# Kernel tuning notes

Hardware: AMD Instinct MI355X
Metric: run time of the kernel (lower is better)

## Reference

```python
import jax, jax.numpy as jnp
import numpy as np

B, D, C = 16384, 2048, 1000  # batch, in_features (feature dim), out_features (classes)
INIT_SCALE = 10.0
EPS = 1e-12


def setup_inputs() -> dict:
    key = jax.random.key(0)
    k1, k2 = jax.random.split(key)
    x = jax.random.normal(k1, (B, D), dtype=jnp.float32)
    weights = jax.random.normal(k2, (C, D), dtype=jnp.float32)  # prototypes
    scales = jnp.ones((1,), dtype=jnp.float32) * INIT_SCALE
    return {"x": x, "weights": weights, "scales": scales}


def reference(x, weights, scales):
    # Pairwise Euclidean distance between features [B,D] and prototypes [C,D]
    x2 = jnp.sum(x * x, axis=-1, keepdims=True)            # [B,1]
    w2 = jnp.sum(weights * weights, axis=-1)               # [C]
    cross = jnp.einsum('bd,cd->bc', x, weights)            # [B,C]
    d2 = jnp.maximum(x2 + w2[None, :] - 2.0 * cross, EPS)  # clamp for sqrt stability
    distances = jnp.sqrt(d2)                               # [B,C]
    logits = -scales * distances  # dml forward: -self.learn(distances)
    return logits
```

## Files before the change

### kernel.cpp

```cpp
#include <hip/hip_runtime.h>
#include <hip/hip_bf16.h>
#include <stdint.h>

#define B_ROWS 16384
#define D_K    2048
#define C_COLS 1000
#define C_PAD  1024
#define EPS_D2 1e-12f

typedef __attribute__((ext_vector_type(8))) short bf16x8;
typedef __attribute__((ext_vector_type(4))) float f32x4;

__device__ __forceinline__ unsigned short f2bf_rne(float f) {
    union { float f; uint32_t u; } a; a.f = f;
    uint32_t u = a.u;
    uint32_t r = (u + 0x7FFFu + ((u >> 16) & 1u)) >> 16;
    return (unsigned short)r;
}

__device__ __forceinline__ void async16(void* lds, const void* g) {
    __builtin_amdgcn_global_load_lds(
        (const __attribute__((address_space(1))) unsigned int*)g,
        (__attribute__((address_space(3))) unsigned int*)lds,
        16, 0, 0);
}

__global__ void prep_kernel(const float* __restrict__ x, const float* __restrict__ w,
                            __hip_bfloat16* __restrict__ xb, __hip_bfloat16* __restrict__ wb,
                            float* __restrict__ x2, float* __restrict__ w2) {
    const int row = blockIdx.x;
    const int t = threadIdx.x;

    const float* src;
    __hip_bfloat16* dst;
    float* norm_out;
    bool valid;
    if (row < B_ROWS) {
        src = x + (size_t)row * D_K;
        dst = xb + (size_t)row * D_K;
        norm_out = x2 + row;
        valid = true;
    } else {
        int c = row - B_ROWS;
        src = w + (size_t)c * D_K;
        dst = wb + (size_t)c * D_K;
        norm_out = w2 + c;
        valid = (c < C_COLS);
    }

    float4 v0, v1;
    if (valid) {
        const float4* s4 = (const float4*)src;
        v0 = s4[t];
        v1 = s4[t + 256];
    } else {
        v0 = make_float4(0.f, 0.f, 0.f, 0.f);
        v1 = v0;
    }

    float ss = v0.x*v0.x + v0.y*v0.y + v0.z*v0.z + v0.w*v0.w
             + v1.x*v1.x + v1.y*v1.y + v1.z*v1.z + v1.w*v1.w;

    uint2 p0, p1;
    p0.x = (uint32_t)f2bf_rne(v0.x) | ((uint32_t)f2bf_rne(v0.y) << 16);
    p0.y = (uint32_t)f2bf_rne(v0.z) | ((uint32_t)f2bf_rne(v0.w) << 16);
    p1.x = (uint32_t)f2bf_rne(v1.x) | ((uint32_t)f2bf_rne(v1.y) << 16);
    p1.y = (uint32_t)f2bf_rne(v1.z) | ((uint32_t)f2bf_rne(v1.w) << 16);
    ((uint2*)dst)[t]       = p0;
    ((uint2*)dst)[t + 256] = p1;

    #pragma unroll
    for (int off = 32; off > 0; off >>= 1) ss += __shfl_down(ss, off, 64);
    __shared__ float wsum[4];
    if ((t & 63) == 0) wsum[t >> 6] = ss;
    __syncthreads();
    if (t == 0) *norm_out = wsum[0] + wsum[1] + wsum[2] + wsum[3];
}

__global__ __launch_bounds__(256) void dml_gemm(
    const __hip_bfloat16* __restrict__ A,
    const __hip_bfloat16* __restrict__ Bm,
    const float* __restrict__ x2, const float* __restrict__ w2,
    const float* __restrict__ scales, float* __restrict__ out)
{
    __shared__ __align__(16) __hip_bfloat16 lsA[128 * 32];
    __shared__ __align__(16) __hip_bfloat16 lsB[128 * 32];

    const int tid  = threadIdx.x;
    const int wave = tid >> 6;
    const int lane = tid & 63;
    const int m0 = blockIdx.y * 128;
    const int n0 = blockIdx.x * 128;
    const int wm = wave >> 1;
    const int wn = wave & 1;

    const int srow = wave * 32 + (lane >> 2);
    const int scol = (lane & 3) * 8;
    const __hip_bfloat16* gA0 = A  + (size_t)(m0 + srow) * D_K + scol;
    const __hip_bfloat16* gA1 = gA0 + (size_t)16 * D_K;
    const __hip_bfloat16* gB0 = Bm + (size_t)(n0 + srow) * D_K + scol;
    const __hip_bfloat16* gB1 = gB0 + (size_t)16 * D_K;
    char* lA0 = (char*)lsA + wave * 32 * 64 + lane * 16;
    char* lA1 = lA0 + 16 * 64;
    char* lB0 = (char*)lsB + wave * 32 * 64 + lane * 16;
    char* lB1 = lB0 + 16 * 64;

    const int fr = lane & 15;
    const int fq = lane >> 4;
    const __hip_bfloat16* fA = lsA + (wm * 64 + fr) * 32 + fq * 8;
    const __hip_bfloat16* fB = lsB + (wn * 64 + fr) * 32 + fq * 8;

    f32x4 acc[4][4] = {};

    for (int k0 = 0; k0 < D_K; k0 += 32) {
        __syncthreads();
        async16(lA0, gA0); async16(lA1, gA1);
        async16(lB0, gB0); async16(lB1, gB1);
        gA0 += 32; gA1 += 32; gB0 += 32; gB1 += 32;
        __syncthreads();

        bf16x8 a[4], b[4];
        #pragma unroll
        for (int i = 0; i < 4; i++) a[i] = *(const bf16x8*)(fA + i * 16 * 32);
        #pragma unroll
        for (int j = 0; j < 4; j++) b[j] = *(const bf16x8*)(fB + j * 16 * 32);
        #pragma unroll
        for (int i = 0; i < 4; i++)
            #pragma unroll
            for (int j = 0; j < 4; j++)
                acc[i][j] = __builtin_amdgcn_mfma_f32_16x16x32_bf16(a[i], b[j], acc[i][j], 0, 0, 0);
    }

    const float s = scales[0];
    const int colb = n0 + wn * 64 + fr;
    const int rowb = m0 + wm * 64 + fq * 4;

    float xv[4][4];
    #pragma unroll
    for (int i = 0; i < 4; i++)
        #pragma unroll
        for (int r = 0; r < 4; r++)
            xv[i][r] = x2[rowb + i * 16 + r];

    #pragma unroll
    for (int j = 0; j < 4; j++) {
        const int gn = colb + j * 16;
        const bool nok = (gn < C_COLS);
        const float w2v = nok ? w2[gn] : 0.f;
        #pragma unroll
        for (int i = 0; i < 4; i++) {
            const int gm = rowb + i * 16;
            #pragma unroll
            for (int r = 0; r < 4; r++) {
                float d2 = xv[i][r] + w2v - 2.0f * acc[i][j][r];
                d2 = fmaxf(d2, EPS_D2);
                float val = -s * __builtin_sqrtf(d2);
                if (nok) out[(size_t)(gm + r) * C_COLS + gn] = val;
            }
        }
    }
}

extern "C" void kernel_launch(void* const* d_in, const int* in_sizes, int n_in,
                              void* d_out, int out_size, void* d_ws, size_t ws_size,
                              hipStream_t stream) {
    const float* x      = (const float*)d_in[0];
    const float* w      = (const float*)d_in[1];
    const float* scales = (const float*)d_in[2];
    float* out = (float*)d_out;

    char* ws = (char*)d_ws;
    __hip_bfloat16* xb = (__hip_bfloat16*)ws;
    __hip_bfloat16* wb = (__hip_bfloat16*)(ws + (size_t)B_ROWS * D_K * 2);
    float* x2 = (float*)(ws + (size_t)B_ROWS * D_K * 2 + (size_t)C_PAD * D_K * 2);
    float* w2 = x2 + B_ROWS;

    prep_kernel<<<dim3(B_ROWS + C_PAD), dim3(256), 0, stream>>>(x, w, xb, wb, x2, w2);
    dml_gemm<<<dim3(C_PAD / 128, B_ROWS / 128), dim3(256), 0, stream>>>(xb, wb, x2, w2, scales, out);
}
```

Before: 327.5 us.

## Swizzle LDS tiles, remap blocks per XCD, and use one wave per prep row

Adds an XOR swizzle to the LDS column slot so the MFMA fragment reads from LDS hit different banks. It also remaps block IDs so that consecutive blocks on the same XCD share A rows, which is meant to improve L2 reuse. The prep kernel now handles one row per wave instead of one per block, which removes the LDS reduction and the __syncthreads. The swizzle has to match on both the global-load side and the fragment-read side; it does, but the logic is subtle.

After: 320.1 us. 1.02x faster.

```diff
diff --git a/kernel.cpp b/kernel.cpp
--- a/kernel.cpp
+++ b/kernel.cpp
@@ -25,11 +25,14 @@
         16, 0, 0);
 }
 
-__global__ void prep_kernel(const float* __restrict__ x, const float* __restrict__ w,
-                            __hip_bfloat16* __restrict__ xb, __hip_bfloat16* __restrict__ wb,
-                            float* __restrict__ x2, float* __restrict__ w2) {
-    const int row = blockIdx.x;
+__global__ __launch_bounds__(256) void prep_kernel(
+    const float* __restrict__ x, const float* __restrict__ w,
+    __hip_bfloat16* __restrict__ xb, __hip_bfloat16* __restrict__ wb,
+    float* __restrict__ x2, float* __restrict__ w2) {
     const int t = threadIdx.x;
+    const int wave = t >> 6;
+    const int lane = t & 63;
+    const int row = blockIdx.x * 4 + wave;
 
     const float* src;
     __hip_bfloat16* dst;
@@ -48,33 +51,30 @@
         valid = (c < C_COLS);
     }
 
-    float4 v0, v1;
+    float4 v[8];
     if (valid) {
         const float4* s4 = (const float4*)src;
-        v0 = s4[t];
-        v1 = s4[t + 256];
+        #pragma unroll
+        for (int i = 0; i < 8; i++) v[i] = s4[lane + 64 * i];
     } else {
-        v0 = make_float4(0.f, 0.f, 0.f, 0.f);
-        v1 = v0;
+        #pragma unroll
+        for (int i = 0; i < 8; i++) v[i] = make_float4(0.f, 0.f, 0.f, 0.f);
     }
 
-    float ss = v0.x*v0.x + v0.y*v0.y + v0.z*v0.z + v0.w*v0.w
-             + v1.x*v1.x + v1.y*v1.y + v1.z*v1.z + v1.w*v1.w;
-
-    uint2 p0, p1;
-    p0.x = (uint32_t)f2bf_rne(v0.x) | ((uint32_t)f2bf_rne(v0.y) << 16);
-    p0.y = (uint32_t)f2bf_rne(v0.z) | ((uint32_t)f2bf_rne(v0.w) << 16);
-    p1.x = (uint32_t)f2bf_rne(v1.x) | ((uint32_t)f2bf_rne(v1.y) << 16);
-    p1.y = (uint32_t)f2bf_rne(v1.z) | ((uint32_t)f2bf_rne(v1.w) << 16);
-    ((uint2*)dst)[t]       = p0;
-    ((uint2*)dst)[t + 256] = p1;
+    float ss = 0.f;
+    uint2* d2p = (uint2*)dst;
+    #pragma unroll
+    for (int i = 0; i < 8; i++) {
+        ss += v[i].x * v[i].x + v[i].y * v[i].y + v[i].z * v[i].z + v[i].w * v[i].w;
+        uint2 p;
+        p.x = (uint32_t)f2bf_rne(v[i].x) | ((uint32_t)f2bf_rne(v[i].y) << 16);
+        p.y = (uint32_t)f2bf_rne(v[i].z) | ((uint32_t)f2bf_rne(v[i].w) << 16);
+        d2p[lane + 64 * i] = p;
+    }
 
     #pragma unroll
     for (int off = 32; off > 0; off >>= 1) ss += __shfl_down(ss, off, 64);
-    __shared__ float wsum[4];
-    if ((t & 63) == 0) wsum[t >> 6] = ss;
-    __syncthreads();
-    if (t == 0) *norm_out = wsum[0] + wsum[1] + wsum[2] + wsum[3];
+    if (lane == 0 && valid) *norm_out = ss;
 }
 
 __global__ __launch_bounds__(256) void dml_gemm(
@@ -89,13 +89,20 @@
     const int tid  = threadIdx.x;
     const int wave = tid >> 6;
     const int lane = tid & 63;
-    const int m0 = blockIdx.y * 128;
-    const int n0 = blockIdx.x * 128;
+
+    const int id  = blockIdx.y * 8 + blockIdx.x;
+    const int xcd = id & 7;
+    const int j   = id >> 3;
+    const int m0  = (xcd * 16 + (j >> 3)) * 128;
+    const int n0  = (j & 7) * 128;
+
     const int wm = wave >> 1;
     const int wn = wave & 1;
 
     const int srow = wave * 32 + (lane >> 2);
-    const int scol = (lane & 3) * 8;
+    const int slot = lane & 3;
+    const int ssw  = (srow >> 1) & 3;
+    const int scol = (slot ^ ssw) * 8;
     const __hip_bfloat16* gA0 = A  + (size_t)(m0 + srow) * D_K + scol;
     const __hip_bfloat16* gA1 = gA0 + (size_t)16 * D_K;
     const __hip_bfloat16* gB0 = Bm + (size_t)(n0 + srow) * D_K + scol;
@@ -105,10 +112,11 @@
     char* lB0 = (char*)lsB + wave * 32 * 64 + lane * 16;
     char* lB1 = lB0 + 16 * 64;
 
-    const int fr = lane & 15;
-    const int fq = lane >> 4;
-    const __hip_bfloat16* fA = lsA + (wm * 64 + fr) * 32 + fq * 8;
-    const __hip_bfloat16* fB = lsB + (wn * 64 + fr) * 32 + fq * 8;
+    const int fr  = lane & 15;
+    const int fq  = lane >> 4;
+    const int fsw = (fr >> 1) & 3;
+    const __hip_bfloat16* fA = lsA + (wm * 64 + fr) * 32 + (fq ^ fsw) * 8;
+    const __hip_bfloat16* fB = lsB + (wn * 64 + fr) * 32 + (fq ^ fsw) * 8;
 
     f32x4 acc[4][4] = {};
 
@@ -123,12 +131,12 @@
         #pragma unroll
         for (int i = 0; i < 4; i++) a[i] = *(const bf16x8*)(fA + i * 16 * 32);
         #pragma unroll
-        for (int j = 0; j < 4; j++) b[j] = *(const bf16x8*)(fB + j * 16 * 32);
+        for (int j2 = 0; j2 < 4; j2++) b[j2] = *(const bf16x8*)(fB + j2 * 16 * 32);
         #pragma unroll
         for (int i = 0; i < 4; i++)
             #pragma unroll
-            for (int j = 0; j < 4; j++)
-                acc[i][j] = __builtin_amdgcn_mfma_f32_16x16x32_bf16(a[i], b[j], acc[i][j], 0, 0, 0);
+            for (int j2 = 0; j2 < 4; j2++)
+                acc[i][j2] = __builtin_amdgcn_mfma_f32_16x16x32_bf16(a[i], b[j2], acc[i][j2], 0, 0, 0);
     }
 
     const float s = scales[0];
@@ -143,8 +151,8 @@
             xv[i][r] = x2[rowb + i * 16 + r];
 
     #pragma unroll
-    for (int j = 0; j < 4; j++) {
-        const int gn = colb + j * 16;
+    for (int j2 = 0; j2 < 4; j2++) {
+        const int gn = colb + j2 * 16;
         const bool nok = (gn < C_COLS);
         const float w2v = nok ? w2[gn] : 0.f;
         #pragma unroll
@@ -152,7 +160,7 @@
             const int gm = rowb + i * 16;
             #pragma unroll
             for (int r = 0; r < 4; r++) {
-                float d2 = xv[i][r] + w2v - 2.0f * acc[i][j][r];
+                float d2 = xv[i][r] + w2v - 2.0f * acc[i][j2][r];
                 d2 = fmaxf(d2, EPS_D2);
                 float val = -s * __builtin_sqrtf(d2);
                 if (nok) out[(size_t)(gm + r) * C_COLS + gn] = val;
@@ -175,6 +183,6 @@
     float* x2 = (float*)(ws + (size_t)B_ROWS * D_K * 2 + (size_t)C_PAD * D_K * 2);
     float* w2 = x2 + B_ROWS;
 
-    prep_kernel<<<dim3(B_ROWS + C_PAD), dim3(256), 0, stream>>>(x, w, xb, wb, x2, w2);
-    dml_gemm<<<dim3(C_PAD / 128, B_ROWS / 128), dim3(256), 0, stream>>>(xb, wb, x2, w2, scales, out);
+    prep_kernel<<<dim3((B_ROWS + C_PAD) / 4), dim3(256), 0, stream>>>(x, w, xb, wb, x2, w2);
+    dml_gemm<<<dim3(8, B_ROWS / 128), dim3(256), 0, stream>>>(xb, wb, x2, w2, scales, out);
 }
```
